# Kernel tuning notes

Measured on AMD Instinct MI355X. Metric: run time of the kernel, lower is better.

Reference implementation:

```python
import jax, jax.numpy as jnp
import numpy as np

NUM_HEADS = 8
NUM_GROUPS = 32
EPS = 1e-5


def setup_inputs() -> dict:
    key = jax.random.key(0)
    k1, k2, k3 = jax.random.split(key, 3)
    B, C, H, W = 2, 512, 64, 64
    x = jax.random.normal(k1, (B, C, H, W), dtype=jnp.float32)
    gn_weight = jnp.ones((C,), dtype=jnp.float32)
    gn_bias = jnp.zeros((C,), dtype=jnp.float32)
    # small init so softmax logits are well-conditioned
    w_qkv = jax.random.normal(k2, (3 * C, C), dtype=jnp.float32) * 0.02
    w_proj = jax.random.normal(k3, (C, C), dtype=jnp.float32) * 0.02
    b_proj = jnp.zeros((C,), dtype=jnp.float32)
    return {"x": x, "gn_weight": gn_weight, "gn_bias": gn_bias,
            "w_qkv": w_qkv, "w_proj": w_proj, "b_proj": b_proj}


def group_norm(x, weight, bias):
    B, C, H, W = x.shape
    xg = x.reshape(B, NUM_GROUPS, C // NUM_GROUPS, H, W)
    mean = xg.mean(axis=(2, 3, 4), keepdims=True)
    var = xg.var(axis=(2, 3, 4), keepdims=True)
    xg = (xg - mean) * jax.lax.rsqrt(var + EPS)
    x = xg.reshape(B, C, H, W)
    return x * weight[None, :, None, None] + bias[None, :, None, None]


def reference(x, gn_weight, gn_bias, w_qkv, w_proj, b_proj):
    B, C, H, W = x.shape
    nh = NUM_HEADS
    hd = C // nh
    N = H * W

    h = group_norm(x, gn_weight, gn_bias)
    # 1x1 conv == per-pixel matmul: [B,3C,H,W]
    qkv = jnp.einsum('bchw,oc->bohw', h, w_qkv)
    # (B,3,nh,hd,N) -> (3,B,nh,N,hd)
    qkv = qkv.reshape(B, 3, nh, hd, N).transpose(1, 0, 2, 4, 3)
    q, k, v = qkv[0], qkv[1], qkv[2]

    scale = hd ** -0.5
    attn = jax.nn.softmax(jnp.einsum('bhnd,bhmd->bhnm', q, k) * scale, axis=-1)
    out = jnp.einsum('bhnm,bhmd->bhnd', attn, v)  # [B,nh,N,hd]
    out = out.transpose(0, 1, 3, 2).reshape(B, C, H, W)
    out = jnp.einsum('bchw,oc->bohw', out, w_proj) + b_proj[None, :, None, None]
    return x + out
```

## Files before the change

### kernel.cpp

```cpp
#include <hip/hip_runtime.h>
#include <math.h>

#define BB 2
#define CC 512
#define NN 4096
#define NH 8
#define HD 64
#define NG 32
#define CPG 16

typedef __attribute__((ext_vector_type(8))) short short8;
typedef __attribute__((ext_vector_type(4))) float f32x4;
typedef __attribute__((ext_vector_type(2))) unsigned int u32x2;

typedef __attribute__((address_space(1))) void glb_t;
typedef __attribute__((address_space(3))) void lds_t;

__device__ __forceinline__ void async16(const void* g, void* l) {
  __builtin_amdgcn_global_load_lds((const glb_t*)g, (lds_t*)l, 16, 0, 0);
}

__device__ __forceinline__ unsigned short f2bf(float f) {
  unsigned int u = __float_as_uint(f);
  u += 0x7fffu + ((u >> 16) & 1u);
  return (unsigned short)(u >> 16);
}

__device__ __forceinline__ unsigned int cvt_pk_bf16(float a, float b) {
  unsigned int r;
  asm("v_cvt_pk_bf16_f32 %0, %1, %2" : "=v"(r) : "v"(a), "v"(b));
  return r;
}

__global__ __launch_bounds__(256) void k_gnstats(const float* __restrict__ x,
                                                 float* __restrict__ stats) {
  int b = blockIdx.x >> 5, g = blockIdx.x & 31;
  const float4* p = (const float4*)(x + (size_t)(b * CC + g * CPG) * NN);
  double s = 0.0, sq = 0.0;
  for (int i = threadIdx.x; i < (CPG * NN) / 4; i += 256) {
    float4 v = p[i];
    s  += (double)v.x + (double)v.y + (double)v.z + (double)v.w;
    sq += (double)v.x * v.x + (double)v.y * v.y + (double)v.z * v.z + (double)v.w * v.w;
  }
  __shared__ double red[512];
  red[threadIdx.x] = s; red[256 + threadIdx.x] = sq;
  __syncthreads();
  for (int off = 128; off > 0; off >>= 1) {
    if (threadIdx.x < off) {
      red[threadIdx.x] += red[threadIdx.x + off];
      red[256 + threadIdx.x] += red[256 + threadIdx.x + off];
    }
    __syncthreads();
  }
  if (threadIdx.x == 0) {
    double mean = red[0] / (double)(CPG * NN);
    double var  = red[256] / (double)(CPG * NN) - mean * mean;
    stats[(b * NG + g) * 2]     = (float)mean;
    stats[(b * NG + g) * 2 + 1] = (float)(1.0 / sqrt(var + 1e-5));
  }
}

__global__ __launch_bounds__(256) void k_gnapply(const float* __restrict__ x,
                                                 const float* __restrict__ gw,
                                                 const float* __restrict__ gb,
                                                 const float* __restrict__ stats,
                                                 unsigned short* __restrict__ hT) {
  int bid = blockIdx.x;
  int b = bid >> 9;
  int c0 = ((bid >> 6) & 7) * 64;
  int n0 = (bid & 63) * 64;
  __shared__ float tile[64 * 65];
  int t = threadIdx.x;
#pragma unroll
  for (int i = 0; i < 16; ++i) {
    int e = i * 256 + t, c = e >> 6, n = e & 63;
    int cg = c0 + c, g = cg >> 4;
    float mu = stats[(b * NG + g) * 2], rs = stats[(b * NG + g) * 2 + 1];
    float v = x[(size_t)(b * CC + cg) * NN + n0 + n];
    tile[c * 65 + n] = (v - mu) * rs * gw[cg] + gb[cg];
  }
  __syncthreads();
#pragma unroll
  for (int i = 0; i < 16; ++i) {
    int e = i * 256 + t, n = e >> 6, c = e & 63;
    hT[(size_t)(b * NN + n0 + n) * CC + c0 + c] = f2bf(tile[c * 65 + n]);
  }
}

__global__ __launch_bounds__(256) void k_cvt(const float* __restrict__ src,
                                             unsigned short* __restrict__ dst) {
  int i = (blockIdx.x * 256 + threadIdx.x) * 4;
  float4 v = *(const float4*)(src + i);
  ushort4 o;
  o.x = f2bf(v.x); o.y = f2bf(v.y); o.z = f2bf(v.z); o.w = f2bf(v.w);
  *(ushort4*)(dst + i) = o;
}

__device__ __forceinline__ void gemm_mainloop(const unsigned short* __restrict__ A,
                                              const unsigned short* __restrict__ Bm,
                                              char* smem, int m0, int n0,
                                              f32x4 acc[4][4]) {
  const int t = threadIdx.x, wave = t >> 6, lane = t & 63;
  const int l15 = lane & 15, lhi = lane >> 4;
  const int wr = wave >> 1, wc = wave & 1;
  const f32x4 fz = {0.f, 0.f, 0.f, 0.f};
#pragma unroll
  for (int mi = 0; mi < 4; ++mi)
#pragma unroll
    for (int ni = 0; ni < 4; ++ni) acc[mi][ni] = fz;

  for (int kt = 0; kt < 8; ++kt) {
    __syncthreads();
#pragma unroll
    for (int issue = 0; issue < 4; ++issue) {
      int slot = issue * 256 + t;
      int row = slot >> 3, g = slot & 7;
      async16(A + (size_t)(m0 + row) * 512 + kt * 64 + g * 8,
              smem + issue * 4096 + wave * 1024);
      async16(Bm + (size_t)(n0 + row) * 512 + kt * 64 + g * 8,
              smem + 16384 + issue * 4096 + wave * 1024);
    }
    __syncthreads();
#pragma unroll
    for (int kk = 0; kk < 2; ++kk) {
      short8 a[4], bf[4];
#pragma unroll
      for (int mi = 0; mi < 4; ++mi)
        a[mi] = *(const short8*)(smem + (wr * 64 + mi * 16 + l15) * 128 + kk * 64 + lhi * 16);
#pragma unroll
      for (int ni = 0; ni < 4; ++ni)
        bf[ni] = *(const short8*)(smem + 16384 + (wc * 64 + ni * 16 + l15) * 128 + kk * 64 + lhi * 16);
#pragma unroll
      for (int mi = 0; mi < 4; ++mi)
#pragma unroll
        for (int ni = 0; ni < 4; ++ni)
          acc[mi][ni] = __builtin_amdgcn_mfma_f32_16x16x32_bf16(a[mi], bf[ni], acc[mi][ni], 0, 0, 0);
    }
  }
}

__global__ __launch_bounds__(256) void k_qkvgemm(const unsigned short* __restrict__ hT,
                                                 const unsigned short* __restrict__ Wq,
                                                 unsigned short* __restrict__ qkv) {
  __shared__ char smem[32768];
  f32x4 acc[4][4];
  int m0 = blockIdx.x * 128, n0 = blockIdx.y * 128;
  gemm_mainloop(hT, Wq, smem, m0, n0, acc);
  const int t = threadIdx.x, wave = t >> 6, lane = t & 63;
  const int l15 = lane & 15, lhi = lane >> 4;
  const int wr = wave >> 1, wc = wave & 1;
#pragma unroll
  for (int mi = 0; mi < 4; ++mi)
#pragma unroll
    for (int ni = 0; ni < 4; ++ni)
#pragma unroll
      for (int r = 0; r < 4; ++r) {
        int m = m0 + wr * 64 + mi * 16 + lhi * 4 + r;
        int o = n0 + wc * 64 + ni * 16 + l15;
        qkv[(size_t)m * 1536 + o] = f2bf(acc[mi][ni][r]);
      }
}

__global__ __launch_bounds__(256) void k_vtrans(const unsigned short* __restrict__ qkv,
                                                unsigned short* __restrict__ vT) {
  int bid = blockIdx.x;
  int bh = bid >> 6, n0 = (bid & 63) * 64;
  int b = bh >> 3, h = bh & 7;
  __shared__ unsigned short tile[64 * 65];
  int t = threadIdx.x;
#pragma unroll
  for (int i = 0; i < 16; ++i) {
    int e = i * 256 + t, n = e >> 6, d = e & 63;
    tile[d * 65 + n] = qkv[(size_t)(b * NN + n0 + n) * 1536 + 1024 + h * 64 + d];
  }
  __syncthreads();
#pragma unroll
  for (int i = 0; i < 16; ++i) {
    int e = i * 256 + t, d = e >> 6, n = e & 63;
    vT[(size_t)(bh * 64 + d) * NN + n0 + n] = tile[d * 65 + n];
  }
}

__global__ __launch_bounds__(256) void k_attn(const unsigned short* __restrict__ qkv,
                                              const unsigned short* __restrict__ vT,
                                              unsigned short* __restrict__ att) {
  __shared__ char smem[32768];
  char* Qs = smem;
  char* Ks = smem + 8192;
  char* Vs = smem + 16384;
  char* Ps = smem + 24576;
  const int t = threadIdx.x, wave = t >> 6, lane = t & 63;
  const int l15 = lane & 15, lhi = lane >> 4;
  int bid0 = blockIdx.x;
  int bid = (bid0 & 7) * 128 + (bid0 >> 3);
  int bh = bid >> 6, q0 = (bid & 63) * 64;
  int b = bh >> 3, h = bh & 7;
  const float C = 0.125f * 1.4426950408889634f;

#pragma unroll
  for (int issue = 0; issue < 2; ++issue) {
    int slot = issue * 256 + t, row = slot >> 3, g = slot & 7;
    async16(qkv + (size_t)(b * NN + q0 + row) * 1536 + h * 64 + ((g ^ (row & 7)) * 8),
            Qs + issue * 4096 + wave * 1024);
  }
  __syncthreads();
  short8 qa[2];
  {
    int rowf = wave * 16 + l15;
#pragma unroll
    for (int kk2 = 0; kk2 < 2; ++kk2)
      qa[kk2] = *(const short8*)(Qs + rowf * 128 + (((kk2 * 4 + lhi) ^ (rowf & 7)) * 16));
  }
  const f32x4 fz = {0.f, 0.f, 0.f, 0.f};
  f32x4 o[4];
#pragma unroll
  for (int ni = 0; ni < 4; ++ni) o[ni] = fz;
  float m = -INFINITY, l = 0.f, mC = 0.f;
  const int prow = wave * 16 + l15;
  const int swz = (l15 & 7) << 4;

  for (int kv0 = 0; kv0 < NN; kv0 += 64) {
    __syncthreads();
#pragma unroll
    for (int issue = 0; issue < 2; ++issue) {
      int slot = issue * 256 + t, row = slot >> 3, g = slot & 7;
      async16(qkv + (size_t)(b * NN + kv0 + row) * 1536 + 512 + h * 64 + ((g ^ (row & 7)) * 8),
              Ks + issue * 4096 + wave * 1024);
      async16(vT + (size_t)(bh * 64 + row) * NN + kv0 + ((g ^ (row & 7)) * 8),
              Vs + issue * 4096 + wave * 1024);
    }
    __syncthreads();

    f32x4 sT[4];
#pragma unroll
    for (int ni = 0; ni < 4; ++ni) sT[ni] = fz;
#pragma unroll
    for (int kk2 = 0; kk2 < 2; ++kk2)
#pragma unroll
      for (int ni = 0; ni < 4; ++ni) {
        int rowf = ni * 16 + l15;
        short8 kb = *(const short8*)(Ks + rowf * 128 + (((kk2 * 4 + lhi) ^ (rowf & 7)) * 16));
        sT[ni] = __builtin_amdgcn_mfma_f32_16x16x32_bf16(kb, qa[kk2], sT[ni], 0, 0, 0);
      }

    float pm = fmaxf(fmaxf(fmaxf(sT[0][0], sT[0][1]), fmaxf(sT[0][2], sT[0][3])),
                     fmaxf(fmaxf(sT[1][0], sT[1][1]), fmaxf(sT[1][2], sT[1][3])));
    pm = fmaxf(pm, fmaxf(fmaxf(fmaxf(sT[2][0], sT[2][1]), fmaxf(sT[2][2], sT[2][3])),
                         fmaxf(fmaxf(sT[3][0], sT[3][1]), fmaxf(sT[3][2], sT[3][3]))));
    pm = fmaxf(pm, __shfl_xor(pm, 16, 64));
    pm = fmaxf(pm, __shfl_xor(pm, 32, 64));

    if (!__all(pm <= m + 32.f)) {
      float nm = fmaxf(m, pm);
      float al = __builtin_amdgcn_exp2f(C * (m - nm));
#pragma unroll
      for (int ni = 0; ni < 4; ++ni)
#pragma unroll
        for (int r = 0; r < 4; ++r) o[ni][r] *= al;
      l *= al;
      m = nm; mC = m * C;
    }

    float ssum = 0.f;
#pragma unroll
    for (int ni = 0; ni < 4; ++ni) {
      float p0 = __builtin_amdgcn_exp2f(__builtin_fmaf(sT[ni][0], C, -mC));
      float p1 = __builtin_amdgcn_exp2f(__builtin_fmaf(sT[ni][1], C, -mC));
      float p2 = __builtin_amdgcn_exp2f(__builtin_fmaf(sT[ni][2], C, -mC));
      float p3 = __builtin_amdgcn_exp2f(__builtin_fmaf(sT[ni][3], C, -mC));
      ssum += (p0 + p1) + (p2 + p3);
      u32x2 pk;
      pk[0] = cvt_pk_bf16(p0, p1);
      pk[1] = cvt_pk_bf16(p2, p3);
      *(u32x2*)(Ps + prow * 128 + ((ni * 32 + lhi * 8) ^ swz)) = pk;
    }
    ssum += __shfl_xor(ssum, 16, 64);
    ssum += __shfl_xor(ssum, 32, 64);
    l += ssum;

#pragma unroll
    for (int kk2 = 0; kk2 < 2; ++kk2) {
      short8 pb = *(const short8*)(Ps + prow * 128 + ((kk2 * 64 + lhi * 16) ^ swz));
#pragma unroll
      for (int ni = 0; ni < 4; ++ni) {
        int rowv = ni * 16 + l15;
        short8 vb = *(const short8*)(Vs + rowv * 128 + (((kk2 * 4 + lhi) ^ (rowv & 7)) * 16));
        o[ni] = __builtin_amdgcn_mfma_f32_16x16x32_bf16(vb, pb, o[ni], 0, 0, 0);
      }
    }
  }

  float rl = 1.f / l;
  size_t base = (size_t)(b * NN + q0 + wave * 16 + l15) * CC + h * 64;
#pragma unroll
  for (int ni = 0; ni < 4; ++ni) {
    u32x2 w;
    w[0] = cvt_pk_bf16(o[ni][0] * rl, o[ni][1] * rl);
    w[1] = cvt_pk_bf16(o[ni][2] * rl, o[ni][3] * rl);
    *(u32x2*)(att + base + ni * 16 + lhi * 4) = w;
  }
}

__global__ __launch_bounds__(256) void k_projgemm(const unsigned short* __restrict__ att,
                                                  const unsigned short* __restrict__ Wp,
                                                  const float* __restrict__ x,
                                                  const float* __restrict__ bproj,
                                                  float* __restrict__ out) {
  __shared__ char smem[33280];
  f32x4 acc[4][4];
  int m0 = blockIdx.x * 128, n0 = blockIdx.y * 128;
  gemm_mainloop(att, Wp, smem, m0, n0, acc);
  const int t = threadIdx.x, wave = t >> 6, lane = t & 63;
  const int l15 = lane & 15, lhi = lane >> 4;
  const int wr = wave >> 1, wc = wave & 1;
  __syncthreads();
  float* stg = (float*)(smem + wave * 8320);
  int b = m0 >> 12;
  int nbase = (m0 & 4095) + wr * 64;
#pragma unroll
  for (int half = 0; half < 2; ++half) {
#pragma unroll
    for (int nl = 0; nl < 2; ++nl) {
      int ni = half * 2 + nl;
#pragma unroll
      for (int mi = 0; mi < 4; ++mi)
#pragma unroll
        for (int r = 0; r < 4; ++r) {
          int cl = nl * 16 + l15;
          int row = mi * 16 + lhi * 4 + r;
          stg[cl * 65 + row] = acc[mi][ni][r];
        }
    }
#pragma unroll 4
    for (int i = 0; i < 32; ++i) {
      int oc = n0 + wc * 64 + half * 32 + i;
      float v = stg[i * 65 + lane];
      size_t idx = (size_t)(b * CC + oc) * NN + nbase + lane;
      out[idx] = x[idx] + v + bproj[oc];
    }
    __syncthreads();
  }
}

extern "C" void kernel_launch(void* const* d_in, const int* in_sizes, int n_in,
                              void* d_out, int out_size, void* d_ws, size_t ws_size,
                              hipStream_t stream) {
  const float* x     = (const float*)d_in[0];
  const float* gw    = (const float*)d_in[1];
  const float* gb    = (const float*)d_in[2];
  const float* wqkv  = (const float*)d_in[3];
  const float* wproj = (const float*)d_in[4];
  const float* bproj = (const float*)d_in[5];
  float* out = (float*)d_out;
  char* ws = (char*)d_ws;

  unsigned short* qkvb  = (unsigned short*)(ws + 0);
  unsigned short* vTb   = (unsigned short*)(ws + 25165824);
  unsigned short* attb  = (unsigned short*)(ws + 33554432);
  unsigned short* hTb   = (unsigned short*)(ws + 41943040);
  unsigned short* wqkvb = (unsigned short*)(ws + 50331648);
  unsigned short* wprojb= (unsigned short*)(ws + 51904512);
  float*          stats = (float*)(ws + 52428800);

  k_gnstats<<<64, 256, 0, stream>>>(x, stats);
  k_gnapply<<<1024, 256, 0, stream>>>(x, gw, gb, stats, hTb);
  k_cvt<<<768, 256, 0, stream>>>(wqkv, wqkvb);
  k_cvt<<<256, 256, 0, stream>>>(wproj, wprojb);
  k_qkvgemm<<<dim3(64, 12), 256, 0, stream>>>(hTb, wqkvb, qkvb);
  k_vtrans<<<1024, 256, 0, stream>>>(qkvb, vTb);
  k_attn<<<1024, 256, 0, stream>>>(qkvb, vTb, attb);
  k_projgemm<<<dim3(64, 4), 256, 0, stream>>>(attb, wprojb, x, bproj, out);
}
```

Baseline: 270.6 us.

## Double-buffer K/V tiles in attention kernel with prefetch and MFMA priority

The attention loop now holds two K/V buffers in LDS. It issues async loads for the next 64-key tile before computing on the current one, and uses one barrier per iteration instead of two, so global-to-LDS latency overlaps with the MFMA and softmax work. It also raises wave priority around the MFMA blocks and adds an 8-byte swizzle bit to the P tile, split into two 8-byte reads, to cut LDS bank conflicts. The cost is more LDS per block (40 KB), a redundant wrap-around prefetch on the last iteration, and reliance on the barrier to wait for the outstanding async loads.

```diff
diff --git a/kernel.cpp b/kernel.cpp
--- a/kernel.cpp
+++ b/kernel.cpp
@@ -184,11 +184,8 @@
 __global__ __launch_bounds__(256) void k_attn(const unsigned short* __restrict__ qkv,
                                               const unsigned short* __restrict__ vT,
                                               unsigned short* __restrict__ att) {
-  __shared__ char smem[32768];
-  char* Qs = smem;
-  char* Ks = smem + 8192;
-  char* Vs = smem + 16384;
-  char* Ps = smem + 24576;
+  __shared__ char smem[40960];
+  char* Ps = smem + 32768;
   const int t = threadIdx.x, wave = t >> 6, lane = t & 63;
   const int l15 = lane & 15, lhi = lane >> 4;
   int bid0 = blockIdx.x;
@@ -200,8 +197,13 @@
 #pragma unroll
   for (int issue = 0; issue < 2; ++issue) {
     int slot = issue * 256 + t, row = slot >> 3, g = slot & 7;
-    async16(qkv + (size_t)(b * NN + q0 + row) * 1536 + h * 64 + ((g ^ (row & 7)) * 8),
-            Qs + issue * 4096 + wave * 1024);
+    int gs = (g ^ (row & 7)) * 8;
+    async16(qkv + (size_t)(b * NN + q0 + row) * 1536 + h * 64 + gs,
+            Ps + issue * 4096 + wave * 1024);
+    async16(qkv + (size_t)(b * NN + row) * 1536 + 512 + h * 64 + gs,
+            smem + issue * 4096 + wave * 1024);
+    async16(vT + (size_t)(bh * 64 + row) * NN + gs,
+            smem + 8192 + issue * 4096 + wave * 1024);
   }
   __syncthreads();
   short8 qa[2];
@@ -209,31 +211,39 @@
     int rowf = wave * 16 + l15;
 #pragma unroll
     for (int kk2 = 0; kk2 < 2; ++kk2)
-      qa[kk2] = *(const short8*)(Qs + rowf * 128 + (((kk2 * 4 + lhi) ^ (rowf & 7)) * 16));
-  }
+      qa[kk2] = *(const short8*)(Ps + rowf * 128 + (((kk2 * 4 + lhi) ^ (rowf & 7)) * 16));
+  }
+  __syncthreads();
+
   const f32x4 fz = {0.f, 0.f, 0.f, 0.f};
   f32x4 o[4];
 #pragma unroll
   for (int ni = 0; ni < 4; ++ni) o[ni] = fz;
   float m = -INFINITY, l = 0.f, mC = 0.f;
   const int prow = wave * 16 + l15;
-  const int swz = (l15 & 7) << 4;
-
-  for (int kv0 = 0; kv0 < NN; kv0 += 64) {
-    __syncthreads();
+  const int pswz = ((l15 & 7) << 4) | (l15 & 8);
+
+  for (int it = 0; it < 64; ++it) {
+    char* Ks = smem + (it & 1) * 16384;
+    char* Vs = Ks + 8192;
+    char* Kn = smem + ((it + 1) & 1) * 16384;
+    char* Vn = Kn + 8192;
+    int kvn = ((it + 1) & 63) * 64;
+
 #pragma unroll
     for (int issue = 0; issue < 2; ++issue) {
       int slot = issue * 256 + t, row = slot >> 3, g = slot & 7;
-      async16(qkv + (size_t)(b * NN + kv0 + row) * 1536 + 512 + h * 64 + ((g ^ (row & 7)) * 8),
-              Ks + issue * 4096 + wave * 1024);
-      async16(vT + (size_t)(bh * 64 + row) * NN + kv0 + ((g ^ (row & 7)) * 8),
-              Vs + issue * 4096 + wave * 1024);
-    }
-    __syncthreads();
+      int gs = (g ^ (row & 7)) * 8;
+      async16(qkv + (size_t)(b * NN + kvn + row) * 1536 + 512 + h * 64 + gs,
+              Kn + issue * 4096 + wave * 1024);
+      async16(vT + (size_t)(bh * 64 + row) * NN + kvn + gs,
+              Vn + issue * 4096 + wave * 1024);
+    }
 
     f32x4 sT[4];
 #pragma unroll
     for (int ni = 0; ni < 4; ++ni) sT[ni] = fz;
+    __builtin_amdgcn_s_setprio(1);
 #pragma unroll
     for (int kk2 = 0; kk2 < 2; ++kk2)
 #pragma unroll
@@ -242,11 +252,15 @@
         short8 kb = *(const short8*)(Ks + rowf * 128 + (((kk2 * 4 + lhi) ^ (rowf & 7)) * 16));
         sT[ni] = __builtin_amdgcn_mfma_f32_16x16x32_bf16(kb, qa[kk2], sT[ni], 0, 0, 0);
       }
-
-    float pm = fmaxf(fmaxf(fmaxf(sT[0][0], sT[0][1]), fmaxf(sT[0][2], sT[0][3])),
-                     fmaxf(fmaxf(sT[1][0], sT[1][1]), fmaxf(sT[1][2], sT[1][3])));
-    pm = fmaxf(pm, fmaxf(fmaxf(fmaxf(sT[2][0], sT[2][1]), fmaxf(sT[2][2], sT[2][3])),
-                         fmaxf(fmaxf(sT[3][0], sT[3][1]), fmaxf(sT[3][2], sT[3][3]))));
+    __builtin_amdgcn_s_setprio(0);
+
+    float pa0 = fmaxf(fmaxf(sT[0][0], sT[0][1]), sT[0][2]);
+    float pa1 = fmaxf(fmaxf(sT[0][3], sT[1][0]), sT[1][1]);
+    float pa2 = fmaxf(fmaxf(sT[1][2], sT[1][3]), sT[2][0]);
+    float pa3 = fmaxf(fmaxf(sT[2][1], sT[2][2]), sT[2][3]);
+    float pa4 = fmaxf(fmaxf(sT[3][0], sT[3][1]), sT[3][2]);
+    float pm  = fmaxf(fmaxf(fmaxf(pa0, pa1), pa2),
+                      fmaxf(fmaxf(pa3, pa4), sT[3][3]));
     pm = fmaxf(pm, __shfl_xor(pm, 16, 64));
     pm = fmaxf(pm, __shfl_xor(pm, 32, 64));
 
@@ -272,15 +286,20 @@
       u32x2 pk;
       pk[0] = cvt_pk_bf16(p0, p1);
       pk[1] = cvt_pk_bf16(p2, p3);
-      *(u32x2*)(Ps + prow * 128 + ((ni * 32 + lhi * 8) ^ swz)) = pk;
+      *(u32x2*)(Ps + prow * 128 + ((ni * 32 + lhi * 8) ^ pswz)) = pk;
     }
     ssum += __shfl_xor(ssum, 16, 64);
     ssum += __shfl_xor(ssum, 32, 64);
     l += ssum;
 
+    __builtin_amdgcn_s_setprio(1);
 #pragma unroll
     for (int kk2 = 0; kk2 < 2; ++kk2) {
-      short8 pb = *(const short8*)(Ps + prow * 128 + ((kk2 * 64 + lhi * 16) ^ swz));
+      int pb0 = (kk2 * 64 + lhi * 16) ^ pswz;
+      union { short8 s; u32x2 d[2]; } pu;
+      pu.d[0] = *(const u32x2*)(Ps + prow * 128 + pb0);
+      pu.d[1] = *(const u32x2*)(Ps + prow * 128 + (pb0 ^ 8));
+      short8 pb = pu.s;
 #pragma unroll
       for (int ni = 0; ni < 4; ++ni) {
         int rowv = ni * 16 + l15;
@@ -288,6 +307,9 @@
         o[ni] = __builtin_amdgcn_mfma_f32_16x16x32_bf16(vb, pb, o[ni], 0, 0, 0);
       }
     }
+    __builtin_amdgcn_s_setprio(0);
+
+    __syncthreads();
   }
 
   float rl = 1.f / l;
```

New measurement: 261.6 us. 1.03x faster.
